# Optimization experiments

Hardware: AMD Instinct MI355X
Metric: run time of the kernel (lower is better)

Reference implementation:

```python
import jax, jax.numpy as jnp
import numpy as np

C_LIGHT = 1.0
CHUNK = 363  # 35937 = 99 * 363 spatial modes per scan step


def _spatial_mode_sum(r, spatial_kernel):
    # sum_n spatial_kernel[n] * sin(n * r), reduced over modes in chunks so we
    # never materialize the full [N, 35937] sin table.
    M = spatial_kernel.shape[0]
    nn = jnp.arange(M, dtype=r.dtype).reshape(-1, CHUNK)      # [steps, CHUNK]
    kk = spatial_kernel.reshape(-1, CHUNK)                    # [steps, CHUNK]

    def body(acc, nk):
        n_c, k_c = nk
        # [N, CHUNK] @ [CHUNK] -> [N]
        return acc + jnp.sin(r[:, None] * n_c[None, :]) @ k_c, None

    acc, _ = jax.lax.scan(body, jnp.zeros_like(r), (nn, kk))
    return acc


def setup_inputs() -> dict:
    key = jax.random.key(0)
    k1, k2, k3 = jax.random.split(key, 3)
    N = 131072
    M_SPATIAL = 35937   # (2*16+1)**3
    M_TEMPORAL = 33     # 2*16+1
    return {
        "spacetime_coords": jax.random.normal(k1, (N, 4), jnp.float32) * 2.0,
        "spatial_kernel": jax.random.normal(k2, (M_SPATIAL,), jnp.float32) * 0.1,
        "temporal_kernel": jax.random.normal(k3, (M_TEMPORAL,), jnp.float32) * 0.1,
        "mass_parameter": jnp.float32(1.0),
        "coupling_strength": jnp.float32(0.1),
    }


def reference(spacetime_coords, spatial_kernel, temporal_kernel,
              mass_parameter, coupling_strength):
    t = spacetime_coords[..., 0]
    x = spacetime_coords[..., 1]
    y = spacetime_coords[..., 2]
    z = spacetime_coords[..., 3]

    spatial_distance_sq = x * x + y * y + z * z
    temporal_distance_sq = (C_LIGHT * t) ** 2
    interval = temporal_distance_sq - spatial_distance_sq

    timelike = interval > 0
    lightlike = jnp.abs(interval) < 1e-10

    # Retarded Green function on the forward timelike region
    spatial_distance = jnp.sqrt(spatial_distance_sq + 1e-12)
    green = jnp.where(
        timelike & (t > 0),
        coupling_strength * jnp.exp(-mass_parameter * spatial_distance) / spatial_distance,
        jnp.zeros_like(t),
    )
    # enforce_causality mask (timelike | lightlike)
    kernel_values = jnp.where(timelike | lightlike, green, jnp.zeros_like(green))

    # Spatial component: sum_n k_n * sin(n*r) / (r + 1e-6); division factored out
    r = jnp.sqrt(spatial_distance_sq + 1e-12)
    spatial_component = _spatial_mode_sum(r, spatial_kernel) / (r + 1e-6)

    # Temporal component: sum_n k_n * cos((n+1)*0.1 * t) * exp(-0.1*|t|)
    freqs = (jnp.arange(temporal_kernel.shape[0], dtype=t.dtype) + 1.0) * 0.1
    envelope = jnp.exp(-0.1 * jnp.abs(t))
    temporal_component = (jnp.cos(t[:, None] * freqs[None, :]) @ temporal_kernel) * envelope

    total_kernel = kernel_values + spatial_component * temporal_component

    # Future light-cone causality mask
    future_lightcone = (temporal_distance_sq >= spatial_distance_sq) & (t >= 0)
    return jnp.where(future_lightcone, total_kernel, jnp.zeros_like(total_kernel))
```

## Files before the change

kernel.cpp:

```cpp
#include <hip/hip_runtime.h>
#include <math.h>


constexpr int NCHUNK = 64;
constexpr int CH     = 576;
constexpr int MPAD   = NCHUNK * CH + 64;

__global__ __launch_bounds__(256)
void mask_kernel(const float4* __restrict__ coords,
                 const float* __restrict__ massp,
                 const float* __restrict__ coupp,
                 const float* __restrict__ tk,
                 const float* __restrict__ ksp,
                 float* __restrict__ out,
                 int* __restrict__ counter,
                 int* __restrict__ list,
                 float* __restrict__ fw,
                 float* __restrict__ rw,
                 float* __restrict__ kpad,
                 int N, int M, int MT)
{
    int i = blockIdx.x * blockDim.x + threadIdx.x;

    if (i < MPAD) kpad[i] = (i < M) ? ksp[i] : 0.0f;
    if (i >= N) return;

    float4 c = coords[i];
    float t = c.x;
    float rsq = c.y * c.y + c.z * c.z + c.w * c.w;
    float t2  = t * t;
    bool  fl  = (t2 >= rsq) && (t >= 0.0f);
    float r   = sqrtf(rsq + 1e-12f);
    float g   = 0.0f;
    if (fl && (t2 > rsq) && (t > 0.0f))
        g = (*coupp) * __expf(-(*massp) * r) / r;
    out[i] = fl ? g : 0.0f;

    unsigned long long bal = __ballot(fl);
    if (fl) {
        float tb = 0.1f * t;
        float T  = 0.0f;
        for (int m = 1; m <= MT; ++m)
            T = fmaf(tk[m - 1], __cosf(tb * (float)m), T);
        T *= __expf(-0.1f * fabsf(t));
        float f = T / (r + 1e-6f);

        int lane   = threadIdx.x & 63;
        int prefix = __popcll(bal & ((1ull << lane) - 1ull));
        int base   = 0;
        if (prefix == 0)
            base = atomicAdd(counter, __popcll(bal));
        int first = __ffsll(bal) - 1;
        base = __shfl(base, first);
        int pos = base + prefix;
        list[pos] = i;
        fw[pos]   = f;
        rw[pos]   = r;
    }
}

__global__ __launch_bounds__(256)
void mode_kernel(const float* __restrict__ kpad,
                 float* __restrict__ out,
                 const int* __restrict__ counter,
                 const int* __restrict__ list,
                 const float* __restrict__ fw,
                 const float* __restrict__ rw)
{
    int gtid   = blockIdx.x * blockDim.x + threadIdx.x;
    int wave   = gtid >> 6;
    int lane   = threadIdx.x & 63;
    int nwaves = (gridDim.x * blockDim.x) >> 6;

    int count   = __builtin_amdgcn_readfirstlane(*counter);
    int ngroups = (count + 63) >> 6;
    int ngpairs = (ngroups + 1) >> 1;
    int items   = NCHUNK * ngpairs;

    for (int it = wave; it < items; it += nwaves) {
        int chunk = __builtin_amdgcn_readfirstlane(it / ngpairs);
        int gpair = it - chunk * ngpairs;

        int li0 = (gpair * 2 + 0) * 64 + lane;
        int li1 = (gpair * 2 + 1) * 64 + lane;

        bool a0 = (li0 < count), a1 = (li1 < count);
        int   idx0 = 0, idx1 = 0;
        float r0 = 0.0f, f0 = 0.0f, r1 = 0.0f, f1 = 0.0f;
        if (a0) { idx0 = list[li0]; r0 = rw[li0]; f0 = fw[li0]; }
        if (a1) { idx1 = list[li1]; r1 = rw[li1]; f1 = fw[li1]; }

        int n0 = chunk * CH;

        double y0 = (double)n0 * (double)r0;
        double q0d = rint(y0 * 0.15915494309189535);
        float  b0 = (float)(y0 - q0d * 6.283185307179586);
        double y1 = (double)n0 * (double)r1;
        double q1d = rint(y1 * 0.15915494309189535);
        float  b1 = (float)(y1 - q1d * 6.283185307179586);

        float t2c0 = 2.0f * __cosf(8.0f * r0);
        float t2c1 = 2.0f * __cosf(8.0f * r1);

        float sc0[8], sp0[8], acc0[8], sc1[8], sp1[8], acc1[8];
#pragma unroll
        for (int j = 0; j < 8; ++j) {
            sc0[j] = __sinf(fmaf((float)j,       r0, b0));
            sp0[j] = __sinf(fmaf((float)(j - 8), r0, b0));
            sc1[j] = __sinf(fmaf((float)j,       r1, b1));
            sp1[j] = __sinf(fmaf((float)(j - 8), r1, b1));
            acc0[j] = 0.0f;
            acc1[j] = 0.0f;
        }

        const float* kc = kpad + n0;
        float4 cA = *(const float4*)(kc);
        float4 cB = *(const float4*)(kc + 4);
        float4 cC = *(const float4*)(kc + 8);
        float4 cD = *(const float4*)(kc + 12);

        constexpr int DSTEPS = CH / 16;
        for (int s = 0; s < DSTEPS; ++s) {
            const float* kn = kc + 16 * (s + 1);
            float4 nA = *(const float4*)(kn);
            float4 nB = *(const float4*)(kn + 4);
            float4 nC = *(const float4*)(kn + 8);
            float4 nD = *(const float4*)(kn + 12);

            float kv0[8] = {cA.x, cA.y, cA.z, cA.w, cB.x, cB.y, cB.z, cB.w};
            float kv1[8] = {cC.x, cC.y, cC.z, cC.w, cD.x, cD.y, cD.z, cD.w};
#pragma unroll
            for (int j = 0; j < 8; ++j) {
                acc0[j] = fmaf(kv0[j], sc0[j], acc0[j]);
                sp0[j]  = fmaf(t2c0, sc0[j], -sp0[j]);
                acc1[j] = fmaf(kv0[j], sc1[j], acc1[j]);
                sp1[j]  = fmaf(t2c1, sc1[j], -sp1[j]);
            }
#pragma unroll
            for (int j = 0; j < 8; ++j) {
                acc0[j] = fmaf(kv1[j], sp0[j], acc0[j]);
                sc0[j]  = fmaf(t2c0, sp0[j], -sc0[j]);
                acc1[j] = fmaf(kv1[j], sp1[j], acc1[j]);
                sc1[j]  = fmaf(t2c1, sp1[j], -sc1[j]);
            }
            cA = nA; cB = nB; cC = nC; cD = nD;
        }

        float S0 = ((acc0[0] + acc0[1]) + (acc0[2] + acc0[3])) +
                   ((acc0[4] + acc0[5]) + (acc0[6] + acc0[7]));
        float S1 = ((acc1[0] + acc1[1]) + (acc1[2] + acc1[3])) +
                   ((acc1[4] + acc1[5]) + (acc1[6] + acc1[7]));
        if (a0) atomicAdd(&out[idx0], S0 * f0);
        if (a1) atomicAdd(&out[idx1], S1 * f1);
    }
}

__global__ __launch_bounds__(256)
void fallback_kernel(const float4* __restrict__ coords,
                     const float* __restrict__ ksp,
                     const float* __restrict__ tk,
                     const float* __restrict__ massp,
                     const float* __restrict__ coupp,
                     float* __restrict__ out, int N, int M, int MT)
{
    int i = blockIdx.x * blockDim.x + threadIdx.x;
    if (i >= N) return;
    float4 c = coords[i];
    float t = c.x;
    float rsq = c.y * c.y + c.z * c.z + c.w * c.w;
    float t2 = t * t;
    bool fl = (t2 >= rsq) && (t >= 0.0f);
    if (!fl) { out[i] = 0.0f; return; }
    float r = sqrtf(rsq + 1e-12f);
    float g = 0.0f;
    if ((t2 > rsq) && (t > 0.0f)) g = (*coupp) * __expf(-(*massp) * r) / r;
    float T = 0.0f, tb = 0.1f * t;
    for (int m = 1; m <= MT; ++m) T = fmaf(tk[m - 1], __cosf(tb * (float)m), T);
    T *= __expf(-0.1f * fabsf(t));
    float f = T / (r + 1e-6f);
    float S = 0.0f;
    for (int n0 = 0; n0 < M; n0 += 1024) {
        int nh = min(n0 + 1024, M);
        double y = (double)n0 * (double)r;
        double q = rint(y * 0.15915494309189535);
        float base = (float)(y - q * 6.283185307179586);
        float s0 = __sinf(base - r), s1 = __sinf(base);
        float tc = 2.0f * __cosf(r);
        for (int n = n0; n < nh; ++n) {
            S = fmaf(ksp[n], s1, S);
            float nx = fmaf(tc, s1, -s0);
            s0 = s1; s1 = nx;
        }
    }
    out[i] = g + S * f;
}

extern "C" void kernel_launch(void* const* d_in, const int* in_sizes, int n_in,
                              void* d_out, int out_size, void* d_ws, size_t ws_size,
                              hipStream_t stream)
{
    const float4* coords = (const float4*)d_in[0];
    const float*  ksp    = (const float*)d_in[1];
    const float*  tk     = (const float*)d_in[2];
    const float*  massp  = (const float*)d_in[3];
    const float*  coupp  = (const float*)d_in[4];
    float*        out    = (float*)d_out;

    int N  = in_sizes[0] / 4;
    int M  = in_sizes[1];
    int MT = in_sizes[2];

    size_t off_list = 16;
    size_t off_fw   = off_list + (size_t)N * 4;
    size_t off_rw   = off_fw   + (size_t)N * 4;
    size_t off_k    = off_rw   + (size_t)N * 4;
    size_t needed   = off_k    + (size_t)MPAD * 4;

    if (ws_size < needed || M > NCHUNK * CH) {
        fallback_kernel<<<(N + 255) / 256, 256, 0, stream>>>(
            coords, ksp, tk, massp, coupp, out, N, M, MT);
        return;
    }

    int*   counter = (int*)d_ws;
    int*   list    = (int*)((char*)d_ws + off_list);
    float* fw      = (float*)((char*)d_ws + off_fw);
    float* rw      = (float*)((char*)d_ws + off_rw);
    float* kpad    = (float*)((char*)d_ws + off_k);

    hipMemsetAsync(d_ws, 0, 16, stream);

    int nthreads = (N > MPAD) ? N : MPAD;
    mask_kernel<<<(nthreads + 255) / 256, 256, 0, stream>>>(
        coords, massp, coupp, tk, ksp, out, counter, list, fw, rw, kpad, N, M, MT);

    mode_kernel<<<2048, 256, 0, stream>>>(kpad, out, counter, list, fw, rw);
}
```

Measured before the change: 125.0 us.

## Assign one spatial-mode chunk per block and stage its kernel coefficients in LDS

The mode kernel now gives each block a fixed chunk (16 blocks per chunk, grid of 1024) instead of a grid-stride loop over (chunk, pair) items. The chunk's coefficients are loaded once into shared memory and read from LDS in the inner loop instead of global/scalar loads. This removes repeated global coefficient traffic and per-item division. In exchange the grid shrinks from 2048 blocks, which may reduce load balance, and it adds a block barrier.

New measurement: 139.0 us. 11.2% more time.

```diff
diff --git a/kernel.cpp b/kernel.cpp
--- a/kernel.cpp
+++ b/kernel.cpp
@@ -5,6 +5,8 @@
 constexpr int NCHUNK = 64;
 constexpr int CH     = 576;
 constexpr int MPAD   = NCHUNK * CH + 64;
+constexpr int BPC    = 16;
+constexpr int DSTEPS = CH / 16;
 
 __global__ __launch_bounds__(256)
 void mask_kernel(const float4* __restrict__ coords,
@@ -67,22 +69,26 @@
                  const float* __restrict__ fw,
                  const float* __restrict__ rw)
 {
-    int gtid   = blockIdx.x * blockDim.x + threadIdx.x;
-    int wave   = gtid >> 6;
-    int lane   = threadIdx.x & 63;
-    int nwaves = (gridDim.x * blockDim.x) >> 6;
+    __shared__ float kch[CH + 16];
+
+    int tid   = threadIdx.x;
+    int lane  = tid & 63;
+    int w     = tid >> 6;
+    int chunk = __builtin_amdgcn_readfirstlane(blockIdx.x / BPC);
+    int lb    = blockIdx.x - chunk * BPC;
+
+    if (tid < (CH + 16) / 4)
+        ((float4*)kch)[tid] = ((const float4*)(kpad + chunk * CH))[tid];
+    __syncthreads();
 
     int count   = __builtin_amdgcn_readfirstlane(*counter);
     int ngroups = (count + 63) >> 6;
     int ngpairs = (ngroups + 1) >> 1;
-    int items   = NCHUNK * ngpairs;
-
-    for (int it = wave; it < items; it += nwaves) {
-        int chunk = __builtin_amdgcn_readfirstlane(it / ngpairs);
-        int gpair = it - chunk * ngpairs;
-
-        int li0 = (gpair * 2 + 0) * 64 + lane;
-        int li1 = (gpair * 2 + 1) * 64 + lane;
+    int n0      = chunk * CH;
+
+    for (int p = lb * 4 + w; p < ngpairs; p += BPC * 4) {
+        int li0 = (p * 2) * 64 + lane;
+        int li1 = li0 + 64;
 
         bool a0 = (li0 < count), a1 = (li1 < count);
         int   idx0 = 0, idx1 = 0;
@@ -90,14 +96,10 @@
         if (a0) { idx0 = list[li0]; r0 = rw[li0]; f0 = fw[li0]; }
         if (a1) { idx1 = list[li1]; r1 = rw[li1]; f1 = fw[li1]; }
 
-        int n0 = chunk * CH;
-
         double y0 = (double)n0 * (double)r0;
-        double q0d = rint(y0 * 0.15915494309189535);
-        float  b0 = (float)(y0 - q0d * 6.283185307179586);
+        float  b0 = (float)(y0 - rint(y0 * 0.15915494309189535) * 6.283185307179586);
         double y1 = (double)n0 * (double)r1;
-        double q1d = rint(y1 * 0.15915494309189535);
-        float  b1 = (float)(y1 - q1d * 6.283185307179586);
+        float  b1 = (float)(y1 - rint(y1 * 0.15915494309189535) * 6.283185307179586);
 
         float t2c0 = 2.0f * __cosf(8.0f * r0);
         float t2c1 = 2.0f * __cosf(8.0f * r1);
@@ -113,19 +115,13 @@
             acc1[j] = 0.0f;
         }
 
-        const float* kc = kpad + n0;
-        float4 cA = *(const float4*)(kc);
-        float4 cB = *(const float4*)(kc + 4);
-        float4 cC = *(const float4*)(kc + 8);
-        float4 cD = *(const float4*)(kc + 12);
-
-        constexpr int DSTEPS = CH / 16;
+        const float4* lk = (const float4*)kch;
+        float4 cA = lk[0], cB = lk[1], cC = lk[2], cD = lk[3];
+
+#pragma unroll 1
         for (int s = 0; s < DSTEPS; ++s) {
-            const float* kn = kc + 16 * (s + 1);
-            float4 nA = *(const float4*)(kn);
-            float4 nB = *(const float4*)(kn + 4);
-            float4 nC = *(const float4*)(kn + 8);
-            float4 nD = *(const float4*)(kn + 12);
+            float4 nA = lk[4 * s + 4], nB = lk[4 * s + 5];
+            float4 nC = lk[4 * s + 6], nD = lk[4 * s + 7];
 
             float kv0[8] = {cA.x, cA.y, cA.z, cA.w, cB.x, cB.y, cB.z, cB.w};
             float kv1[8] = {cC.x, cC.y, cC.z, cC.w, cD.x, cD.y, cD.z, cD.w};
@@ -234,5 +230,5 @@
     mask_kernel<<<(nthreads + 255) / 256, 256, 0, stream>>>(
         coords, massp, coupp, tk, ksp, out, counter, list, fw, rw, kpad, N, M, MT);
 
-    mode_kernel<<<2048, 256, 0, stream>>>(kpad, out, counter, list, fw, rw);
-}
+    mode_kernel<<<NCHUNK * BPC, 256, 0, stream>>>(kpad, out, counter, list, fw, rw);
+}
```
